# Optimization experiments

Measured on AMD Instinct MI355X. Metric: run time of the kernel, lower is better.

## Reference

```python
import jax, jax.numpy as jnp
import numpy as np

# Dims: B nodes, Z species (elements), IN/OUT channels, M = 2*l+1 (l=1)
B, Z, IN, OUT, M = 8192, 10, 512, 512, 3
ALPHA = 1.0 / np.sqrt(IN)  # self.alpha = 1/sqrt(in_dim)
SQRT3 = float(np.sqrt(3.0))


def setup_inputs() -> dict:
    key = jax.random.key(0)
    k1, k2, k3 = jax.random.split(key, 3)
    t = jax.random.normal(k1, (B, IN, M), dtype=jnp.float32)
    species = jax.random.randint(k2, (B,), 0, Z)
    node_attrs = jax.nn.one_hot(species, Z, dtype=jnp.float32)  # [B, Z] one-hot
    # torch.nn.init.uniform_(weights, -sqrt(3), sqrt(3))
    weights = jax.random.uniform(k3, (Z, OUT, IN), dtype=jnp.float32,
                                 minval=-SQRT3, maxval=SQRT3)
    return {"t": t, "node_attrs": node_attrs, "weights": weights}


def reference(t, node_attrs, weights):
    # Faithful to: einsum('bz, zCc, bcd -> bCd', node_attrs, weights*alpha, t)
    # Contract weights with t first per species ([Z,B,C,M], ~500MB), which
    # avoids the huge [B,C,c] per-node weight-gather intermediate, then
    # select/sum over species with the one-hot node_attrs.
    W = weights * ALPHA                       # [Z, OUT, IN]
    zt = jnp.einsum('zCc,bcd->zbCd', W, t)    # [Z, B, OUT, M]
    out = jnp.einsum('bz,zbCd->bCd', node_attrs, zt)  # [B, OUT, M]
    return out
```

## Files before the change

kernel.cpp:

```cpp
#include <hip/hip_runtime.h>
#include <stdint.h>

#define NB   8192
#define NZ   10
#define CIN  512
#define COUT 512
#define MM   3
#define ALPHA 0.04419417382415922f

#define BM 32
#define BN 64
#define BK 32
#define KITERS (CIN / BK)
#define MAX_MTILES 266

typedef short bf16x8 __attribute__((ext_vector_type(8)));
typedef float f32x4  __attribute__((ext_vector_type(4)));

__device__ __forceinline__ uint16_t f2bf(float f) {
    union { float f; uint32_t i; } v; v.f = f;
    uint32_t x = v.i;
    x += 0x7fffu + ((x >> 16) & 1u);
    return (uint16_t)(x >> 16);
}
__device__ __forceinline__ uint32_t pack2(float a, float b) {
    return (uint32_t)f2bf(a) | ((uint32_t)f2bf(b) << 16);
}

__global__ __launch_bounds__(256)
void decode_kernel(const float* __restrict__ attrs, int* __restrict__ species) {
    int b = blockIdx.x * 256 + threadIdx.x;
    if (b >= NB) return;
    const float* a = attrs + (size_t)b * NZ;
    int s = 0;
    #pragma unroll
    for (int z = 0; z < NZ; z++) if (a[z] > 0.5f) s = z;
    species[b] = s;
}

__global__ __launch_bounds__(256)
void sort_kernel(const int* __restrict__ species, int* __restrict__ sorted,
                 int* __restrict__ offsets, int* __restrict__ tile_offsets) {
    __shared__ int cnt[NZ];
    __shared__ int cur[NZ];
    const int tid = threadIdx.x;
    if (tid < NZ) cnt[tid] = 0;
    __syncthreads();
    for (int i = tid; i < NB; i += 256) atomicAdd(&cnt[species[i]], 1);
    __syncthreads();
    if (tid == 0) {
        int off = 0, toff = 0;
        for (int z = 0; z < NZ; z++) {
            offsets[z] = off;
            tile_offsets[z] = toff;
            cur[z] = off;
            off  += cnt[z];
            toff += (cnt[z] + BM - 1) / BM;
        }
        offsets[NZ] = off;
        tile_offsets[NZ] = toff;
    }
    __syncthreads();
    for (int i = tid; i < NB; i += 256) {
        int s = species[i];
        int pos = atomicAdd(&cur[s], 1);
        sorted[pos] = i;
    }
}

__global__ __launch_bounds__(256)
void gemm_kernel(const float* __restrict__ t, const float* __restrict__ w,
                 const int* __restrict__ sorted, const int* __restrict__ offsets,
                 const int* __restrict__ tile_offsets, float* __restrict__ out) {
    __shared__ ushort As[MM][BM][BK + 8];
    __shared__ ushort Bs[BN][BK + 8];
    __shared__ int snode[BM];

    const int tz = blockIdx.x;
    if (tz >= tile_offsets[NZ]) return;
    int z = 0;
    #pragma unroll
    for (int i = 1; i < NZ; i++) if (tile_offsets[i] <= tz) z = i;

    const int seg_start = offsets[z];
    const int seg_end   = offsets[z + 1];
    const int m_base    = seg_start + (tz - tile_offsets[z]) * BM;
    const int tid = threadIdx.x;

    if (tid < BM) {
        int pos = m_base + tid;
        snode[tid] = sorted[min(pos, seg_end - 1)];
    }
    __syncthreads();

    const int Cbase = blockIdx.y * BN;

    const int aNode = tid >> 3, aPart = tid & 7;
    const int bRow  = tid >> 2, bPart = tid & 3;
    const float* tnode = t + (size_t)snode[aNode] * (CIN * MM) + aPart * 12;
    const float* wrow  = w + ((size_t)z * COUT + Cbase + bRow) * CIN + bPart * 8;

    const int wv = tid >> 6, lane = tid & 63;
    const int wm = wv & 1, wn = wv >> 1;
    const int q = lane >> 4, mr = lane & 15;

    f32x4 acc[MM][2];
    #pragma unroll
    for (int d = 0; d < MM; d++)
        #pragma unroll
        for (int s2 = 0; s2 < 2; s2++)
            acc[d][s2] = (f32x4){0.f, 0.f, 0.f, 0.f};

    for (int kt = 0; kt < KITERS; kt++) {
        const int c0 = kt * BK;
        const float4* asrc = (const float4*)(tnode + c0 * MM);
        float4 f0 = asrc[0], f1 = asrc[1], f2 = asrc[2];
        float v[12] = {f0.x, f0.y, f0.z, f0.w, f1.x, f1.y, f1.z, f1.w,
                       f2.x, f2.y, f2.z, f2.w};
        #pragma unroll
        for (int d = 0; d < MM; d++) {
            uint2 wq;
            wq.x = pack2(v[d],     v[d + 3]);
            wq.y = pack2(v[d + 6], v[d + 9]);
            *(uint2*)&As[d][aNode][aPart * 4] = wq;
        }
        const float4* bsrc = (const float4*)(wrow + c0);
        float4 g0 = bsrc[0], g1 = bsrc[1];
        uint4 bw;
        bw.x = pack2(g0.x, g0.y); bw.y = pack2(g0.z, g0.w);
        bw.z = pack2(g1.x, g1.y); bw.w = pack2(g1.z, g1.w);
        *(uint4*)&Bs[bRow][bPart * 8] = bw;
        __syncthreads();

        bf16x8 af[MM], bfr[2];
        #pragma unroll
        for (int d = 0; d < MM; d++)
            af[d] = *(const bf16x8*)&As[d][wm * 16 + mr][q * 8];
        #pragma unroll
        for (int s2 = 0; s2 < 2; s2++)
            bfr[s2] = *(const bf16x8*)&Bs[wn * 32 + s2 * 16 + mr][q * 8];
        #pragma unroll
        for (int d = 0; d < MM; d++)
            #pragma unroll
            for (int s2 = 0; s2 < 2; s2++)
                acc[d][s2] = __builtin_amdgcn_mfma_f32_16x16x32_bf16(
                    af[d], bfr[s2], acc[d][s2], 0, 0, 0);
        __syncthreads();
    }

    #pragma unroll
    for (int s2 = 0; s2 < 2; s2++) {
        const int Cg = Cbase + wn * 32 + s2 * 16 + mr;
        #pragma unroll
        for (int r = 0; r < 4; r++) {
            const int m_local = wm * 16 + q * 4 + r;
            if (m_base + m_local < seg_end) {
                float* o = out + (size_t)snode[m_local] * (COUT * MM) + Cg * MM;
                o[0] = ALPHA * acc[0][s2][r];
                o[1] = ALPHA * acc[1][s2][r];
                o[2] = ALPHA * acc[2][s2][r];
            }
        }
    }
}

extern "C" void kernel_launch(void* const* d_in, const int* in_sizes, int n_in,
                              void* d_out, int out_size, void* d_ws, size_t ws_size,
                              hipStream_t stream) {
    const float* t     = (const float*)d_in[0];
    const float* attrs = (const float*)d_in[1];
    const float* w     = (const float*)d_in[2];
    float* out = (float*)d_out;

    int* species      = (int*)d_ws;
    int* sorted       = species + NB;
    int* offsets      = sorted + NB;
    int* tile_offsets = offsets + 16;

    hipLaunchKernelGGL(decode_kernel, dim3(NB / 256), dim3(256), 0, stream,
                       attrs, species);
    hipLaunchKernelGGL(sort_kernel, dim3(1), dim3(256), 0, stream,
                       species, sorted, offsets, tile_offsets);
    hipLaunchKernelGGL(gemm_kernel, dim3(MAX_MTILES, COUT / BN), dim3(256), 0, stream,
                       t, w, sorted, offsets, tile_offsets, out);
}
```

Measured before the change: 182.7 us.

## Pre-pack inputs to bf16, fold M into rows, and use large async-loaded GEMM tiles

Replaces the single-block species sort with wave-ballot counting and placement kernels, pre-converts t (gathered in species order, transposed so each m-component is a row) and weights to bf16 buffers, and runs a 128x128 tiled MFMA GEMM over 3*B rows using direct global-to-LDS loads. This removes repeated fp32 loading and conversion of t per output-column block, the serial sort, and improves MFMA tile reuse. It adds extra packing passes and workspace traffic, and the unpadded LDS tiles may cause bank conflicts; tail tiles may read beyond the species segment.

```diff
diff --git a/kernel.cpp b/kernel.cpp
--- a/kernel.cpp
+++ b/kernel.cpp
@@ -8,11 +8,12 @@
 #define MM   3
 #define ALPHA 0.04419417382415922f
 
-#define BM 32
-#define BN 64
+#define ROWS_TOTAL (NB * MM)
+#define BM 128
+#define BN 128
 #define BK 32
 #define KITERS (CIN / BK)
-#define MAX_MTILES 266
+#define MAX_MT (ROWS_TOTAL / BM + NZ)
 
 typedef short bf16x8 __attribute__((ext_vector_type(8)));
 typedef float f32x4  __attribute__((ext_vector_type(4)));
@@ -26,55 +27,99 @@
 __device__ __forceinline__ uint32_t pack2(float a, float b) {
     return (uint32_t)f2bf(a) | ((uint32_t)f2bf(b) << 16);
 }
-
-__global__ __launch_bounds__(256)
-void decode_kernel(const float* __restrict__ attrs, int* __restrict__ species) {
-    int b = blockIdx.x * 256 + threadIdx.x;
-    if (b >= NB) return;
+__device__ __forceinline__ void async16(const ushort* g, ushort* l) {
+    __builtin_amdgcn_global_load_lds((const uint32_t*)g, (uint32_t*)l, 16, 0, 0);
+}
+
+__global__ __launch_bounds__(256)
+void decode_count(const float* __restrict__ attrs, int* __restrict__ species,
+                  int* __restrict__ cnt) {
+    const int b = blockIdx.x * 256 + threadIdx.x;
     const float* a = attrs + (size_t)b * NZ;
     int s = 0;
     #pragma unroll
     for (int z = 0; z < NZ; z++) if (a[z] > 0.5f) s = z;
     species[b] = s;
-}
-
-__global__ __launch_bounds__(256)
-void sort_kernel(const int* __restrict__ species, int* __restrict__ sorted,
-                 int* __restrict__ offsets, int* __restrict__ tile_offsets) {
-    __shared__ int cnt[NZ];
-    __shared__ int cur[NZ];
-    const int tid = threadIdx.x;
-    if (tid < NZ) cnt[tid] = 0;
-    __syncthreads();
-    for (int i = tid; i < NB; i += 256) atomicAdd(&cnt[species[i]], 1);
-    __syncthreads();
-    if (tid == 0) {
+    const int lane = threadIdx.x & 63;
+    #pragma unroll
+    for (int z = 0; z < NZ; z++) {
+        unsigned long long m = __ballot(s == z);
+        if (lane == 0 && m) atomicAdd(&cnt[z], __popcll(m));
+    }
+}
+
+__global__ void scan_kernel(const int* __restrict__ cnt, int* __restrict__ offsets,
+                            int* __restrict__ tile_offsets, int* __restrict__ cur) {
+    if (threadIdx.x == 0) {
         int off = 0, toff = 0;
         for (int z = 0; z < NZ; z++) {
-            offsets[z] = off;
-            tile_offsets[z] = toff;
-            cur[z] = off;
+            offsets[z] = off; tile_offsets[z] = toff; cur[z] = off;
             off  += cnt[z];
-            toff += (cnt[z] + BM - 1) / BM;
+            toff += (3 * cnt[z] + BM - 1) / BM;
         }
-        offsets[NZ] = off;
-        tile_offsets[NZ] = toff;
-    }
-    __syncthreads();
-    for (int i = tid; i < NB; i += 256) {
-        int s = species[i];
-        int pos = atomicAdd(&cur[s], 1);
-        sorted[pos] = i;
-    }
-}
-
-__global__ __launch_bounds__(256)
-void gemm_kernel(const float* __restrict__ t, const float* __restrict__ w,
+        offsets[NZ] = off; tile_offsets[NZ] = toff;
+    }
+}
+
+__global__ __launch_bounds__(256)
+void place_kernel(const int* __restrict__ species, int* __restrict__ cur,
+                  int* __restrict__ sorted) {
+    const int b = blockIdx.x * 256 + threadIdx.x;
+    const int s = species[b];
+    const int lane = threadIdx.x & 63;
+    #pragma unroll
+    for (int z = 0; z < NZ; z++) {
+        unsigned long long m = __ballot(s == z);
+        if (s == z) {
+            int leader = __ffsll((unsigned long long)m) - 1;
+            int rank = __popcll(m & ((1ull << lane) - 1ull));
+            int base = 0;
+            if (lane == leader) base = atomicAdd(&cur[z], __popcll(m));
+            base = __shfl(base, leader);
+            sorted[base + rank] = b;
+        }
+    }
+}
+
+__global__ __launch_bounds__(256)
+void pack_t(const float* __restrict__ t, const int* __restrict__ sorted,
+            ushort* __restrict__ tt) {
+    const int w = threadIdx.x >> 6, L = threadIdx.x & 63;
+    const int p = blockIdx.x * 4 + w;
+    const int node = sorted[p];
+    const float4* src = (const float4*)(t + (size_t)node * (CIN * MM) + L * 24);
+    float4 f[6];
+    #pragma unroll
+    for (int i = 0; i < 6; i++) f[i] = src[i];
+    const float* v = (const float*)f;
+    #pragma unroll
+    for (int d = 0; d < MM; d++) {
+        uint4 o;
+        o.x = pack2(v[d],      v[3 + d]);
+        o.y = pack2(v[6 + d],  v[9 + d]);
+        o.z = pack2(v[12 + d], v[15 + d]);
+        o.w = pack2(v[18 + d], v[21 + d]);
+        *(uint4*)&tt[(size_t)(3 * p + d) * CIN + L * 8] = o;
+    }
+}
+
+__global__ __launch_bounds__(256)
+void pack_w(const float* __restrict__ w, ushort* __restrict__ wt) {
+    const int i = (blockIdx.x * 256 + threadIdx.x) * 8;
+    float4 a = *(const float4*)(w + i);
+    float4 b = *(const float4*)(w + i + 4);
+    uint4 o;
+    o.x = pack2(a.x, a.y); o.y = pack2(a.z, a.w);
+    o.z = pack2(b.x, b.y); o.w = pack2(b.z, b.w);
+    *(uint4*)(wt + i) = o;
+}
+
+__global__ __launch_bounds__(256)
+void gemm_kernel(const ushort* __restrict__ tt, const ushort* __restrict__ wt,
                  const int* __restrict__ sorted, const int* __restrict__ offsets,
                  const int* __restrict__ tile_offsets, float* __restrict__ out) {
-    __shared__ ushort As[MM][BM][BK + 8];
-    __shared__ ushort Bs[BN][BK + 8];
-    __shared__ int snode[BM];
+    __shared__ ushort As[BM][BK];
+    __shared__ ushort Bs[BN][BK];
 
     const int tz = blockIdx.x;
     if (tz >= tile_offsets[NZ]) return;
@@ -82,83 +127,70 @@
     #pragma unroll
     for (int i = 1; i < NZ; i++) if (tile_offsets[i] <= tz) z = i;
 
-    const int seg_start = offsets[z];
-    const int seg_end   = offsets[z + 1];
-    const int m_base    = seg_start + (tz - tile_offsets[z]) * BM;
+    const int row_base = 3 * offsets[z] + (tz - tile_offsets[z]) * BM;
+    const int row_end  = 3 * offsets[z + 1];
+    const int Cbase    = blockIdx.y * BN;
+
     const int tid = threadIdx.x;
-
-    if (tid < BM) {
-        int pos = m_base + tid;
-        snode[tid] = sorted[min(pos, seg_end - 1)];
-    }
-    __syncthreads();
-
-    const int Cbase = blockIdx.y * BN;
-
-    const int aNode = tid >> 3, aPart = tid & 7;
-    const int bRow  = tid >> 2, bPart = tid & 3;
-    const float* tnode = t + (size_t)snode[aNode] * (CIN * MM) + aPart * 12;
-    const float* wrow  = w + ((size_t)z * COUT + Cbase + bRow) * CIN + bPart * 8;
-
-    const int wv = tid >> 6, lane = tid & 63;
-    const int wm = wv & 1, wn = wv >> 1;
-    const int q = lane >> 4, mr = lane & 15;
-
-    f32x4 acc[MM][2];
-    #pragma unroll
-    for (int d = 0; d < MM; d++)
-        #pragma unroll
-        for (int s2 = 0; s2 < 2; s2++)
-            acc[d][s2] = (f32x4){0.f, 0.f, 0.f, 0.f};
+    const int w = tid >> 6, L = tid & 63;
+
+    const int lrow = L >> 2;
+    const int lk   = (L & 3) * 8;
+    const ushort* gA = tt + (size_t)(row_base + w * 32 + lrow) * CIN + lk;
+    const ushort* gB = wt + ((size_t)z * COUT + Cbase + w * 32 + lrow) * CIN + lk;
+    ushort* lA0 = &As[w * 32][0];
+    ushort* lA1 = &As[w * 32 + 16][0];
+    ushort* lB0 = &Bs[w * 32][0];
+    ushort* lB1 = &Bs[w * 32 + 16][0];
+
+    const int wm = w & 1, wn = w >> 1;
+    const int q = L >> 4, mr = L & 15;
+
+    f32x4 acc[4][4];
+    #pragma unroll
+    for (int i = 0; i < 4; i++)
+        #pragma unroll
+        for (int j = 0; j < 4; j++) acc[i][j] = (f32x4){0.f, 0.f, 0.f, 0.f};
 
     for (int kt = 0; kt < KITERS; kt++) {
-        const int c0 = kt * BK;
-        const float4* asrc = (const float4*)(tnode + c0 * MM);
-        float4 f0 = asrc[0], f1 = asrc[1], f2 = asrc[2];
-        float v[12] = {f0.x, f0.y, f0.z, f0.w, f1.x, f1.y, f1.z, f1.w,
-                       f2.x, f2.y, f2.z, f2.w};
-        #pragma unroll
-        for (int d = 0; d < MM; d++) {
-            uint2 wq;
-            wq.x = pack2(v[d],     v[d + 3]);
-            wq.y = pack2(v[d + 6], v[d + 9]);
-            *(uint2*)&As[d][aNode][aPart * 4] = wq;
-        }
-        const float4* bsrc = (const float4*)(wrow + c0);
-        float4 g0 = bsrc[0], g1 = bsrc[1];
-        uint4 bw;
-        bw.x = pack2(g0.x, g0.y); bw.y = pack2(g0.z, g0.w);
-        bw.z = pack2(g1.x, g1.y); bw.w = pack2(g1.z, g1.w);
-        *(uint4*)&Bs[bRow][bPart * 8] = bw;
+        const int ko = kt * BK;
+        async16(gA + ko, lA0);
+        async16(gA + (size_t)16 * CIN + ko, lA1);
+        async16(gB + ko, lB0);
+        async16(gB + (size_t)16 * CIN + ko, lB1);
         __syncthreads();
 
-        bf16x8 af[MM], bfr[2];
-        #pragma unroll
-        for (int d = 0; d < MM; d++)
-            af[d] = *(const bf16x8*)&As[d][wm * 16 + mr][q * 8];
-        #pragma unroll
-        for (int s2 = 0; s2 < 2; s2++)
-            bfr[s2] = *(const bf16x8*)&Bs[wn * 32 + s2 * 16 + mr][q * 8];
-        #pragma unroll
-        for (int d = 0; d < MM; d++)
+        bf16x8 af[4], bf[4];
+        #pragma unroll
+        for (int am = 0; am < 4; am++)
+            af[am] = *(const bf16x8*)&As[wm * 64 + am * 16 + mr][q * 8];
+        #pragma unroll
+        for (int bn = 0; bn < 4; bn++)
+            bf[bn] = *(const bf16x8*)&Bs[wn * 64 + bn * 16 + mr][q * 8];
+        #pragma unroll
+        for (int am = 0; am < 4; am++)
             #pragma unroll
-            for (int s2 = 0; s2 < 2; s2++)
-                acc[d][s2] = __builtin_amdgcn_mfma_f32_16x16x32_bf16(
-                    af[d], bfr[s2], acc[d][s2], 0, 0, 0);
+            for (int bn = 0; bn < 4; bn++)
+                acc[am][bn] = __builtin_amdgcn_mfma_f32_16x16x32_bf16(
+                    af[am], bf[bn], acc[am][bn], 0, 0, 0);
         __syncthreads();
     }
 
     #pragma unroll
-    for (int s2 = 0; s2 < 2; s2++) {
-        const int Cg = Cbase + wn * 32 + s2 * 16 + mr;
+    for (int am = 0; am < 4; am++) {
         #pragma unroll
         for (int r = 0; r < 4; r++) {
-            const int m_local = wm * 16 + q * 4 + r;
-            if (m_base + m_local < seg_end) {
-                float* o = out + (size_t)snode[m_local] * (COUT * MM) + Cg * MM;
-                o[0] = ALPHA * acc[0][s2][r];
-                o[1] = ALPHA * acc[1][s2][r];
-                o[2] = ALPHA * acc[2][s2][r];
+            const int Rg = row_base + wm * 64 + am * 16 + q * 4 + r;
+            if (Rg < row_end) {
+                const int pos = Rg / 3;
+                const int d = Rg - 3 * pos;
+                const int node = sorted[pos];
+                float* o = out + (size_t)node * (COUT * MM) + d;
+                #pragma unroll
+                for (int bn = 0; bn < 4; bn++) {
+                    const int Cg = Cbase + wn * 64 + bn * 16 + mr;
+                    o[(size_t)Cg * 3] = ALPHA * acc[am][bn][r];
+                }
             }
         }
     }
@@ -172,15 +204,28 @@
     const float* w     = (const float*)d_in[2];
     float* out = (float*)d_out;
 
-    int* species      = (int*)d_ws;
-    int* sorted       = species + NB;
-    int* offsets      = sorted + NB;
-    int* tile_offsets = offsets + 16;
-
-    hipLaunchKernelGGL(decode_kernel, dim3(NB / 256), dim3(256), 0, stream,
-                       attrs, species);
-    hipLaunchKernelGGL(sort_kernel, dim3(1), dim3(256), 0, stream,
-                       species, sorted, offsets, tile_offsets);
-    hipLaunchKernelGGL(gemm_kernel, dim3(MAX_MTILES, COUT / BN), dim3(256), 0, stream,
-                       t, w, sorted, offsets, tile_offsets, out);
-}
+    uint8_t* ws = (uint8_t*)d_ws;
+    int* species      = (int*)ws;                        ws += NB * 4;
+    int* sorted       = (int*)ws;                        ws += NB * 4;
+    int* cnt          = (int*)ws;                        ws += 16 * 4;
+    int* offsets      = (int*)ws;                        ws += 16 * 4;
+    int* tile_offsets = (int*)ws;                        ws += 16 * 4;
+    int* cur          = (int*)ws;                        ws += 16 * 4;
+    ws = (uint8_t*)(((uintptr_t)ws + 255) & ~(uintptr_t)255);
+    ushort* wt = (ushort*)ws;                            ws += (size_t)NZ * COUT * CIN * 2;
+    ushort* tt = (ushort*)ws;
+
+    hipMemsetAsync(cnt, 0, 16 * 4, stream);
+    hipLaunchKernelGGL(decode_count, dim3(NB / 256), dim3(256), 0, stream,
+                       attrs, species, cnt);
+    hipLaunchKernelGGL(scan_kernel, dim3(1), dim3(64), 0, stream,
+                       cnt, offsets, tile_offsets, cur);
+    hipLaunchKernelGGL(place_kernel, dim3(NB / 256), dim3(256), 0, stream,
+                       species, cur, sorted);
+    hipLaunchKernelGGL(pack_t, dim3(NB / 4), dim3(256), 0, stream,
+                       t, sorted, tt);
+    hipLaunchKernelGGL(pack_w, dim3((NZ * COUT * CIN) / (256 * 8)), dim3(256), 0, stream,
+                       w, wt);
+    hipLaunchKernelGGL(gemm_kernel, dim3(MAX_MT, COUT / BN), dim3(256), 0, stream,
+                       tt, wt, sorted, offsets, tile_offsets, out);
+}
```

Result: slower. 186.5 us (+2.1%).
